# Kernel optimization log

Measured on AMD Instinct MI355X. Metric: run time of the kernel, lower is better.

## Reference

```python
import jax, jax.numpy as jnp
import numpy as np

# IR-Net EDE surrogate-gradient constants (ir_1w1a.IRConv2d defaults)
K = 10.0
T = 0.1
BN_EPS = 1e-5

@jax.custom_vjp
def binary_quantize(x):
    return jnp.sign(x)

def _bq_fwd(x):
    return jnp.sign(x), x

def _bq_bwd(x, g):
    # grad = k * t * (1 - tanh(x*t)^2) * g   (IR-Net BinaryQuantize.backward)
    return (K * T * (1.0 - jnp.tanh(x * T) ** 2) * g,)

binary_quantize.defvjp(_bq_fwd, _bq_bwd)


def setup_inputs() -> dict:
    key = jax.random.key(0)
    k1, k2 = jax.random.split(key, 2)
    return {
        "x": jax.random.normal(k1, (32, 256, 56, 56), dtype=jnp.float32),
        "weight": jax.random.normal(k2, (256, 256, 3, 3), dtype=jnp.float32) * 0.05,
        "gamma": jnp.ones((256,), dtype=jnp.float32),
        "beta": jnp.zeros((256,), dtype=jnp.float32),
    }


def _convalg(x, weight, gamma, beta):
    co = weight.shape[0]
    wf = weight.reshape(co, -1)
    # per-output-channel standardization of weights
    bw = weight - wf.mean(-1).reshape(co, 1, 1, 1)
    std = jnp.std(bw.reshape(co, -1), axis=-1, ddof=1).reshape(co, 1, 1, 1)  # torch unbiased std
    bw = bw / std
    # detached power-of-2 per-channel scale: sw = 2^round(log2(mean|bw|))
    sw = jax.lax.stop_gradient(
        2.0 ** jnp.round(jnp.log2(jnp.abs(bw).reshape(co, -1).mean(-1)))
    ).reshape(co, 1, 1, 1)
    bwq = binary_quantize(bw) * sw   # binarized, scaled weights {-sw, +sw}
    ba = binary_quantize(x)          # binarized activations {-1, +1}
    y = jax.lax.conv_general_dilated(
        ba, bwq,
        window_strides=(1, 1),
        padding=((1, 1), (1, 1)),
        dimension_numbers=("NCHW", "OIHW", "NCHW"),
    )
    # BatchNorm2d, training-mode forward (batch statistics, biased variance)
    mean = y.mean(axis=(0, 2, 3), keepdims=True)
    var = y.var(axis=(0, 2, 3), keepdims=True)
    yn = (y - mean) * jax.lax.rsqrt(var + BN_EPS)
    yn = yn * gamma.reshape(1, -1, 1, 1) + beta.reshape(1, -1, 1, 1)
    # Hardtanh
    return jnp.clip(yn, -1.0, 1.0)


def reference(x, weight, gamma, beta):
    return _convalg(x, weight, gamma, beta)
```

## Files before the change

kernel.cpp:

```cpp
#include <hip/hip_runtime.h>
#include <math.h>

#define HH 56
#define WW 56
#define NB 32
#define CC 256
#define PIX 3136
#define M_TOT 100352
#define PADH 58
#define PADW 58
#define ACTQ_BYTES ((size_t)NB*PADH*PADW*CC)
#define WQ_BYTES ((size_t)9*CC*CC)
#define SBUF_BYTES ((size_t)M_TOT*CC*2)
#define BM 128
#define BN 256

typedef unsigned int u32;
typedef unsigned long long u64;
typedef int v4i __attribute__((ext_vector_type(4)));

typedef const __attribute__((address_space(1))) unsigned int* as1_u32p;
typedef __attribute__((address_space(3))) unsigned int* as3_u32p;
#define GLOAD_LDS16(g, l) \
  __builtin_amdgcn_global_load_lds((as1_u32p)(g), (as3_u32p)(l), 16, 0, 0)

__global__ __launch_bounds__(256) void pack_weights_i8(
    const float* __restrict__ wt, signed char* __restrict__ wq,
    float* __restrict__ swv,
    long long* __restrict__ sumS, long long* __restrict__ sumSS) {
  int co = blockIdx.x;
  int t  = threadIdx.x;
  int lane = t & 63, wid = t >> 6;

  float wv[9];
  const float* wp = wt + ((size_t)co*CC + t)*9;
  double psum = 0.0;
#pragma unroll
  for (int k = 0; k < 9; ++k) { wv[k] = wp[k]; psum += (double)wv[k]; }

  __shared__ double redm[4];
#pragma unroll
  for (int off = 32; off > 0; off >>= 1) psum += __shfl_xor(psum, off);
  if (lane == 0) redm[wid] = psum;
  __syncthreads();
  double mean = (redm[0]+redm[1]+redm[2]+redm[3]) * (1.0/2304.0);

  double pabs = 0.0, psq = 0.0;
#pragma unroll
  for (int k = 0; k < 9; ++k) {
    double d = (double)wv[k] - mean;
    pabs += fabs(d);
    psq  += d*d;
  }
#pragma unroll
  for (int off = 32; off > 0; off >>= 1) {
    pabs += __shfl_xor(pabs, off);
    psq  += __shfl_xor(psq,  off);
  }
  __shared__ double reda[4], redq[4];
  if (lane == 0) { reda[wid] = pabs; redq[wid] = psq; }
  __syncthreads();
  if (t == 0) {
    double sa = reda[0]+reda[1]+reda[2]+reda[3];
    double sq = redq[0]+redq[1]+redq[2]+redq[3];
    double stdv = sqrt(sq / 2303.0);
    double mabs = (sa * (1.0/2304.0)) / stdv;
    swv[co] = (float)exp2(rint(log2(mabs)));
    sumS[co]  = 0;
    sumSS[co] = 0;
  }
#pragma unroll
  for (int k = 0; k < 9; ++k)
    wq[((size_t)k*CC + co)*CC + t] =
        (((double)wv[k] - mean) > 0.0) ? (signed char)1 : (signed char)-1;
}

__global__ __launch_bounds__(256) void pack_acts_i8(
    const float* __restrict__ x, signed char* __restrict__ actq) {
  int n = blockIdx.y, tile = blockIdx.x;
  int lane = threadIdx.x & 63, cw = threadIdx.x >> 6;
  int pp = tile*64 + lane;
  if (pp >= PADH*PADW) return;
  int ph = pp / PADW, pw = pp - ph*PADW;
  signed char* dst = actq + ((size_t)(n*PADH + ph)*PADW + pw)*CC + cw*64;
  if (ph == 0 || ph == PADH-1 || pw == 0 || pw == PADW-1) {
    uint4 z = make_uint4(0u, 0u, 0u, 0u);
#pragma unroll
    for (int q = 0; q < 4; ++q) ((uint4*)dst)[q] = z;
    return;
  }
  int h = ph - 1, w = pw - 1;
  const float* xp = x + ((size_t)(n*CC + cw*64))*PIX + h*WW + w;
  u32 wrd[16];
#pragma unroll
  for (int c16 = 0; c16 < 16; ++c16) {
    u32 v = 0;
#pragma unroll
    for (int b = 0; b < 4; ++b) {
      float f = xp[(size_t)(c16*4 + b)*PIX];
      v |= (f > 0.0f ? 0x01u : 0xFFu) << (8*b);
    }
    wrd[c16] = v;
  }
#pragma unroll
  for (int q = 0; q < 4; ++q)
    ((uint4*)dst)[q] = make_uint4(wrd[4*q], wrd[4*q+1], wrd[4*q+2], wrd[4*q+3]);
}


#define STAGEM(SN, BUF) do {                                              \
    int tn_ = (SN) >> 2, kn_ = (SN) & 3;                                  \
    int aoff_ = ((tn_/3 - 1)*PADW + (tn_%3 - 1))*CC + kn_*64;             \
    int boff_ = tn_*65536 + kn_*64;                                       \
    char* nb_ = (char*)lds + (BUF)*24576;                                 \
    GLOAD_LDS16(pA0 + aoff_, nb_ + ldst);                                 \
    GLOAD_LDS16(pA1 + aoff_, nb_ + 4096 + ldst);                          \
    GLOAD_LDS16(pB0 + boff_, nb_ + 8192 + ldst);                          \
    GLOAD_LDS16(pB1 + boff_, nb_ + 12288 + ldst);                         \
    GLOAD_LDS16(pB2 + boff_, nb_ + 16384 + ldst);                         \
    GLOAD_LDS16(pB3 + boff_, nb_ + 20480 + ldst);                         \
  } while (0)

#define STEPB(S, WTXT, DODMA) do {                                        \
    asm volatile("s_waitcnt " WTXT ::: "memory");                         \
    __builtin_amdgcn_s_barrier();                                         \
    if (DODMA) { STAGEM((S) + 2, ((S) + 2) % 3); }                        \
    const char* cb_ = (const char*)lds + ((S) % 3)*24576;                 \
    v4i af[4], bf[8];                                                     \
    _Pragma("unroll")                                                     \
    for (int i = 0; i < 4; ++i)                                           \
      af[i] = *(const v4i*)(cb_ + (ar0 + i*16 + lm)*64 + rdo);            \
    _Pragma("unroll")                                                     \
    for (int j = 0; j < 8; ++j)                                           \
      bf[j] = *(const v4i*)(cb_ + 8192 + (bc0 + j*16 + lm)*64 + rdo);     \
    __builtin_amdgcn_s_setprio(1);                                        \
    _Pragma("unroll")                                                     \
    for (int i = 0; i < 4; ++i)                                           \
      _Pragma("unroll")                                                   \
      for (int j = 0; j < 8; ++j)                                         \
        acc[i][j] = __builtin_amdgcn_mfma_i32_16x16x64_i8(af[i], bf[j],   \
                                                          acc[i][j], 0, 0, 0); \
    __builtin_amdgcn_s_setprio(0);                                        \
  } while (0)

template <bool S16>
__global__ __launch_bounds__(256, 2) void bconv_mfma(
    const signed char* __restrict__ actq, const signed char* __restrict__ wq,
    short* __restrict__ s16out, float* __restrict__ f32out,
    u64* __restrict__ sumS, u64* __restrict__ sumSS) {
  __shared__ char lds[73728] __attribute__((aligned(16)));
  __shared__ int colS[256], colQ[256];

  int t = threadIdx.x;
  int lane = t & 63, wv = t >> 6;
  int lm = lane & 15, quad = lane >> 4;
  int ar0 = (wv & 1) * 64;
  int bc0 = (wv >> 1) * 128;
  int Mbase = blockIdx.x * BM;

  colS[t] = 0; colQ[t] = 0;

  int r = t >> 2, c16 = t & 3;
  int cs = c16 ^ ((r >> 1) & 3);
  const signed char *pA0, *pA1;
  {
    int P = Mbase + r;
    int n_ = P / PIX, pl_ = P % PIX, h_ = pl_ / WW, w_ = pl_ % WW;
    pA0 = actq + ((size_t)(n_*PADH + h_+1)*PADW + (w_+1))*CC + cs*16;
    P += 64;
    n_ = P / PIX; pl_ = P % PIX; h_ = pl_ / WW; w_ = pl_ % WW;
    pA1 = actq + ((size_t)(n_*PADH + h_+1)*PADW + (w_+1))*CC + cs*16;
  }
  const signed char* pB0 = wq + (size_t)r*CC + cs*16;
  const signed char* pB1 = pB0 +  64*CC;
  const signed char* pB2 = pB0 + 128*CC;
  const signed char* pB3 = pB0 + 192*CC;
  int ldst = t*16;

  int rdo = (quad ^ ((lm >> 1) & 3)) * 16;

  v4i acc[4][8];
#pragma unroll
  for (int i = 0; i < 4; ++i)
#pragma unroll
    for (int j = 0; j < 8; ++j) acc[i][j] = 0;

  STAGEM(0, 0);
  STAGEM(1, 1);

#pragma unroll 1
  for (int s = 0; s < 33; s += 3) {
    STEPB(s,     "vmcnt(6)", true);
    STEPB(s + 1, "vmcnt(6)", true);
    STEPB(s + 2, "vmcnt(6)", true);
  }
  STEPB(33, "vmcnt(6)", true);
  STEPB(34, "vmcnt(6)", false);
  STEPB(35, "vmcnt(0)", false);

  int Sl[8] = {0,0,0,0,0,0,0,0}, Ql[8] = {0,0,0,0,0,0,0,0};
  if (S16) {
    short* tb = s16out + (size_t)blockIdx.x * (BM*BN);
#pragma unroll
    for (int i = 0; i < 4; ++i) {
      int rhat = ar0 + i*16 + quad*4;
#pragma unroll
      for (int j = 0; j < 8; ++j) {
        int colo = bc0 + j*16 + lm;
        v4i a = acc[i][j];
        int2 pk;
        pk.x = (a.x & 0xFFFF) | (a.y << 16);
        pk.y = (a.z & 0xFFFF) | (a.w << 16);
        *(int2*)(tb + (size_t)colo*BM + rhat) = pk;
        Sl[j] += a.x + a.y + a.z + a.w;
        Ql[j] += a.x*a.x + a.y*a.y + a.z*a.z + a.w*a.w;
      }
    }
  } else {
#pragma unroll
    for (int i = 0; i < 4; ++i) {
      int R = Mbase + ar0 + i*16 + quad*4;
      int nR = R / PIX, plR = R % PIX;
#pragma unroll
      for (int j = 0; j < 8; ++j) {
        int colo = bc0 + j*16 + lm;
        v4i a = acc[i][j];
        size_t idx = ((size_t)nR*CC + colo)*PIX + plR;
        *(float4*)(f32out + idx) =
            make_float4((float)a.x, (float)a.y, (float)a.z, (float)a.w);
        Sl[j] += a.x + a.y + a.z + a.w;
        Ql[j] += a.x*a.x + a.y*a.y + a.z*a.z + a.w*a.w;
      }
    }
  }
#pragma unroll
  for (int j = 0; j < 8; ++j) {
    int S = Sl[j], Q = Ql[j];
    S += __shfl_xor(S, 16); S += __shfl_xor(S, 32);
    Q += __shfl_xor(Q, 16); Q += __shfl_xor(Q, 32);
    if (quad == 0) {
      atomicAdd(&colS[bc0 + j*16 + lm], S);
      atomicAdd(&colQ[bc0 + j*16 + lm], Q);
    }
  }
  __syncthreads();
  atomicAdd(&sumS[t], (u64)(long long)colS[t]);
  atomicAdd(&sumSS[t], (u64)(long long)colQ[t]);
}

__global__ void finalize_stats(
    const long long* __restrict__ sumS, const long long* __restrict__ sumSS,
    const float* __restrict__ swv,
    const float* __restrict__ gamma, const float* __restrict__ beta,
    float* __restrict__ AB) {
  int c = threadIdx.x;
  double mu  = (double)sumS[c]  / (double)M_TOT;
  double var = (double)sumSS[c] / (double)M_TOT - mu*mu;
  double sw  = (double)swv[c];
  double inv = 1.0 / sqrt(sw*sw*var + 1e-5);
  double scale = (double)gamma[c] * sw * inv;
  double shift = (double)beta[c] - scale * mu;
  AB[c]      = (float)scale;
  AB[CC + c] = (float)shift;
}

__global__ __launch_bounds__(256) void bn_apply_s16(
    const short* __restrict__ s, float* __restrict__ out,
    const float* __restrict__ AB, int n8) {
  int i = blockIdx.x*256 + threadIdx.x;
  if (i >= n8) return;
  union { int4 v; short sh[8]; } u;
  u.v = ((const int4*)s)[i];
  int base   = i*8;
  int tile   = base >> 15;
  int within = base & 32767;
  int col    = within >> 7;
  int rh     = within & 127;
  int R  = tile*BM + rh;
  int n_ = R / PIX, pl = R % PIX;
  float a = AB[col], b = AB[CC + col];
  float* op = out + ((size_t)n_*CC + col)*PIX + pl;
  float4 o0, o1;
  o0.x = fminf(1.f, fmaxf(-1.f, (float)u.sh[0]*a + b));
  o0.y = fminf(1.f, fmaxf(-1.f, (float)u.sh[1]*a + b));
  o0.z = fminf(1.f, fmaxf(-1.f, (float)u.sh[2]*a + b));
  o0.w = fminf(1.f, fmaxf(-1.f, (float)u.sh[3]*a + b));
  o1.x = fminf(1.f, fmaxf(-1.f, (float)u.sh[4]*a + b));
  o1.y = fminf(1.f, fmaxf(-1.f, (float)u.sh[5]*a + b));
  o1.z = fminf(1.f, fmaxf(-1.f, (float)u.sh[6]*a + b));
  o1.w = fminf(1.f, fmaxf(-1.f, (float)u.sh[7]*a + b));
  ((float4*)op)[0] = o0;
  ((float4*)op)[1] = o1;
}

__global__ __launch_bounds__(256) void bn_apply_f32(
    float* __restrict__ out, const float* __restrict__ AB, int n4) {
  int i = blockIdx.x*256 + threadIdx.x;
  if (i >= n4) return;
  float4 v = ((float4*)out)[i];
  int c = ((i*4) / PIX) & (CC-1);
  float a = AB[c], b = AB[CC + c];
  v.x = fminf(1.f, fmaxf(-1.f, v.x*a + b));
  v.y = fminf(1.f, fmaxf(-1.f, v.y*a + b));
  v.z = fminf(1.f, fmaxf(-1.f, v.z*a + b));
  v.w = fminf(1.f, fmaxf(-1.f, v.w*a + b));
  ((float4*)out)[i] = v;
}

extern "C" void kernel_launch(void* const* d_in, const int* in_sizes, int n_in,
                              void* d_out, int out_size, void* d_ws, size_t ws_size,
                              hipStream_t stream) {
  (void)in_sizes; (void)n_in; (void)out_size;
  const float* x     = (const float*)d_in[0];
  const float* wt    = (const float*)d_in[1];
  const float* gamma = (const float*)d_in[2];
  const float* beta  = (const float*)d_in[3];
  float* out = (float*)d_out;

  char* ws = (char*)d_ws;
  size_t off = 0;
  signed char* actq = (signed char*)(ws + off);
  off += ACTQ_BYTES;             off = (off + 255) & ~(size_t)255;
  signed char* wq = (signed char*)(ws + off);
  off += WQ_BYTES;               off = (off + 255) & ~(size_t)255;
  float* swv = (float*)(ws + off); off += 1024;
  float* AB  = (float*)(ws + off); off += 2048;
  long long* sumS  = (long long*)(ws + off); off += 2048;
  long long* sumSS = (long long*)(ws + off); off += 2048;
  off = (off + 255) & ~(size_t)255;
  short* sbuf = (short*)(ws + off);
  bool s16 = (ws_size >= off + SBUF_BYTES);

  pack_weights_i8<<<256, 256, 0, stream>>>(wt, wq, swv, sumS, sumSS);
  pack_acts_i8<<<dim3(53, NB), 256, 0, stream>>>(x, actq);
  if (s16) {
    bconv_mfma<true><<<dim3(M_TOT/BM, 1), 256, 0, stream>>>(
        actq, wq, sbuf, nullptr, (u64*)sumS, (u64*)sumSS);
  } else {
    bconv_mfma<false><<<dim3(M_TOT/BM, 1), 256, 0, stream>>>(
        actq, wq, nullptr, out, (u64*)sumS, (u64*)sumSS);
  }
  finalize_stats<<<1, 256, 0, stream>>>(sumS, sumSS, swv, gamma, beta, AB);
  if (s16) {
    bn_apply_s16<<<(M_TOT*CC/8 + 255)/256, 256, 0, stream>>>(
        sbuf, out, AB, M_TOT*CC/8);
  } else {
    bn_apply_f32<<<(M_TOT*CC/4 + 255)/256, 256, 0, stream>>>(
        out, AB, M_TOT*CC/4);
  }
}
```

Baseline: 157.9 us.

## Enlarge conv tile to 256x256 with 8 waves and interleaved double-buffer pipeline

Doubles the M tile of the int8 MFMA implicit-GEMM conv to 256 rows with 512 threads (8 waves in a 2x4 grid). The LDS ring changes from triple to double buffering, and A and B staging are split and interleaved with sub-blocks of MFMAs separated by barriers. This aims to raise data reuse per LDS byte and hide global loads behind compute. In exchange it adds many more block-wide barriers per k-step and a full vmcnt(0) drain every iteration, and it updates the bn_apply tile indexing to match.

```diff
diff --git a/kernel.cpp b/kernel.cpp
--- a/kernel.cpp
+++ b/kernel.cpp
@@ -12,7 +12,7 @@
 #define ACTQ_BYTES ((size_t)NB*PADH*PADW*CC)
 #define WQ_BYTES ((size_t)9*CC*CC)
 #define SBUF_BYTES ((size_t)M_TOT*CC*2)
-#define BM 128
+#define BM 256
 #define BN 256
 
 typedef unsigned int u32;
@@ -108,57 +108,22 @@
 }
 
 
-#define STAGEM(SN, BUF) do {                                              \
-    int tn_ = (SN) >> 2, kn_ = (SN) & 3;                                  \
-    int aoff_ = ((tn_/3 - 1)*PADW + (tn_%3 - 1))*CC + kn_*64;             \
-    int boff_ = tn_*65536 + kn_*64;                                       \
-    char* nb_ = (char*)lds + (BUF)*24576;                                 \
-    GLOAD_LDS16(pA0 + aoff_, nb_ + ldst);                                 \
-    GLOAD_LDS16(pA1 + aoff_, nb_ + 4096 + ldst);                          \
-    GLOAD_LDS16(pB0 + boff_, nb_ + 8192 + ldst);                          \
-    GLOAD_LDS16(pB1 + boff_, nb_ + 12288 + ldst);                         \
-    GLOAD_LDS16(pB2 + boff_, nb_ + 16384 + ldst);                         \
-    GLOAD_LDS16(pB3 + boff_, nb_ + 20480 + ldst);                         \
-  } while (0)
-
-#define STEPB(S, WTXT, DODMA) do {                                        \
-    asm volatile("s_waitcnt " WTXT ::: "memory");                         \
-    __builtin_amdgcn_s_barrier();                                         \
-    if (DODMA) { STAGEM((S) + 2, ((S) + 2) % 3); }                        \
-    const char* cb_ = (const char*)lds + ((S) % 3)*24576;                 \
-    v4i af[4], bf[8];                                                     \
-    _Pragma("unroll")                                                     \
-    for (int i = 0; i < 4; ++i)                                           \
-      af[i] = *(const v4i*)(cb_ + (ar0 + i*16 + lm)*64 + rdo);            \
-    _Pragma("unroll")                                                     \
-    for (int j = 0; j < 8; ++j)                                           \
-      bf[j] = *(const v4i*)(cb_ + 8192 + (bc0 + j*16 + lm)*64 + rdo);     \
-    __builtin_amdgcn_s_setprio(1);                                        \
-    _Pragma("unroll")                                                     \
-    for (int i = 0; i < 4; ++i)                                           \
-      _Pragma("unroll")                                                   \
-      for (int j = 0; j < 8; ++j)                                         \
-        acc[i][j] = __builtin_amdgcn_mfma_i32_16x16x64_i8(af[i], bf[j],   \
-                                                          acc[i][j], 0, 0, 0); \
-    __builtin_amdgcn_s_setprio(0);                                        \
-  } while (0)
-
 template <bool S16>
-__global__ __launch_bounds__(256, 2) void bconv_mfma(
+__global__ __launch_bounds__(512, 4) void bconv_mfma(
     const signed char* __restrict__ actq, const signed char* __restrict__ wq,
     short* __restrict__ s16out, float* __restrict__ f32out,
     u64* __restrict__ sumS, u64* __restrict__ sumSS) {
-  __shared__ char lds[73728] __attribute__((aligned(16)));
+  __shared__ char lds[65536] __attribute__((aligned(16)));
   __shared__ int colS[256], colQ[256];
 
   int t = threadIdx.x;
   int lane = t & 63, wv = t >> 6;
   int lm = lane & 15, quad = lane >> 4;
-  int ar0 = (wv & 1) * 64;
-  int bc0 = (wv >> 1) * 128;
+  int wr = wv >> 2;
+  int wc = wv & 3;
   int Mbase = blockIdx.x * BM;
 
-  colS[t] = 0; colQ[t] = 0;
+  if (t < 256) { colS[t] = 0; colQ[t] = 0; }
 
   int r = t >> 2, c16 = t & 3;
   int cs = c16 ^ ((r >> 1) & 3);
@@ -167,46 +132,96 @@
     int P = Mbase + r;
     int n_ = P / PIX, pl_ = P % PIX, h_ = pl_ / WW, w_ = pl_ % WW;
     pA0 = actq + ((size_t)(n_*PADH + h_+1)*PADW + (w_+1))*CC + cs*16;
-    P += 64;
+    P += 128;
     n_ = P / PIX; pl_ = P % PIX; h_ = pl_ / WW; w_ = pl_ % WW;
     pA1 = actq + ((size_t)(n_*PADH + h_+1)*PADW + (w_+1))*CC + cs*16;
   }
   const signed char* pB0 = wq + (size_t)r*CC + cs*16;
-  const signed char* pB1 = pB0 +  64*CC;
-  const signed char* pB2 = pB0 + 128*CC;
-  const signed char* pB3 = pB0 + 192*CC;
+  const signed char* pB1 = pB0 + 128*CC;
   int ldst = t*16;
 
   int rdo = (quad ^ ((lm >> 1) & 3)) * 16;
 
-  v4i acc[4][8];
-#pragma unroll
-  for (int i = 0; i < 4; ++i)
-#pragma unroll
-    for (int j = 0; j < 8; ++j) acc[i][j] = 0;
-
-  STAGEM(0, 0);
-  STAGEM(1, 1);
+  v4i acc[8][4];
+#pragma unroll
+  for (int i = 0; i < 8; ++i)
+#pragma unroll
+    for (int j = 0; j < 4; ++j) acc[i][j] = 0;
+
+#define STAGE_A(SN) do {                                                  \
+    int tn_ = (SN) >> 2, kn_ = (SN) & 3;                                  \
+    int aoff_ = ((tn_/3 - 1)*PADW + (tn_%3 - 1))*CC + kn_*64;             \
+    char* nb_ = (char*)lds + (((SN) & 1) << 15);                          \
+    GLOAD_LDS16(pA0 + aoff_, nb_ + ldst);                                 \
+    GLOAD_LDS16(pA1 + aoff_, nb_ + 8192 + ldst);                          \
+  } while (0)
+#define STAGE_B(SN) do {                                                  \
+    int tn_ = (SN) >> 2, kn_ = (SN) & 3;                                  \
+    int boff_ = tn_*65536 + kn_*64;                                       \
+    char* nb_ = (char*)lds + (((SN) & 1) << 15);                          \
+    GLOAD_LDS16(pB0 + boff_, nb_ + 16384 + ldst);                         \
+    GLOAD_LDS16(pB1 + boff_, nb_ + 24576 + ldst);                         \
+  } while (0)
+#define MFMA8(I0, J0) do {                                                \
+    __builtin_amdgcn_s_setprio(1);                                        \
+    _Pragma("unroll")                                                     \
+    for (int i_ = 0; i_ < 4; ++i_)                                        \
+      _Pragma("unroll")                                                   \
+      for (int j_ = 0; j_ < 2; ++j_)                                      \
+        acc[(I0)+i_][(J0)+j_] = __builtin_amdgcn_mfma_i32_16x16x64_i8(    \
+            af[(I0)+i_], bf[(J0)+j_], acc[(I0)+i_][(J0)+j_], 0, 0, 0);    \
+    __builtin_amdgcn_s_setprio(0);                                        \
+  } while (0)
+
+  STAGE_A(0);
+  STAGE_B(0);
+  asm volatile("s_waitcnt vmcnt(0)" ::: "memory");
+  __builtin_amdgcn_s_barrier();
+  __builtin_amdgcn_sched_barrier(0);
 
 #pragma unroll 1
-  for (int s = 0; s < 33; s += 3) {
-    STEPB(s,     "vmcnt(6)", true);
-    STEPB(s + 1, "vmcnt(6)", true);
-    STEPB(s + 2, "vmcnt(6)", true);
-  }
-  STEPB(33, "vmcnt(6)", true);
-  STEPB(34, "vmcnt(6)", false);
-  STEPB(35, "vmcnt(0)", false);
-
-  int Sl[8] = {0,0,0,0,0,0,0,0}, Ql[8] = {0,0,0,0,0,0,0,0};
+  for (int s = 0; s < 36; ++s) {
+    const char* cb_ = (const char*)lds + ((s & 1) << 15);
+    bool dostage = (s < 35);
+    v4i af[8], bf[4];
+    if (dostage) STAGE_A(s + 1);
+#pragma unroll
+    for (int i = 0; i < 4; ++i)
+      af[i] = *(const v4i*)(cb_ + (wr*128 + i*16 + lm)*64 + rdo);
+#pragma unroll
+    for (int j = 0; j < 2; ++j)
+      bf[j] = *(const v4i*)(cb_ + 16384 + (wc*64 + j*16 + lm)*64 + rdo);
+    __builtin_amdgcn_s_barrier();
+    MFMA8(0, 0);
+    __builtin_amdgcn_s_barrier();
+    if (dostage) STAGE_B(s + 1);
+#pragma unroll
+    for (int j = 2; j < 4; ++j)
+      bf[j] = *(const v4i*)(cb_ + 16384 + (wc*64 + j*16 + lm)*64 + rdo);
+    __builtin_amdgcn_s_barrier();
+    MFMA8(0, 2);
+    __builtin_amdgcn_s_barrier();
+#pragma unroll
+    for (int i = 4; i < 8; ++i)
+      af[i] = *(const v4i*)(cb_ + (wr*128 + i*16 + lm)*64 + rdo);
+    __builtin_amdgcn_s_barrier();
+    MFMA8(4, 0);
+    __builtin_amdgcn_s_barrier();
+    MFMA8(4, 2);
+    asm volatile("s_waitcnt vmcnt(0)" ::: "memory");
+    __builtin_amdgcn_s_barrier();
+    __builtin_amdgcn_sched_barrier(0);
+  }
+
+  int Sl[4] = {0,0,0,0}, Ql[4] = {0,0,0,0};
   if (S16) {
     short* tb = s16out + (size_t)blockIdx.x * (BM*BN);
 #pragma unroll
-    for (int i = 0; i < 4; ++i) {
-      int rhat = ar0 + i*16 + quad*4;
-#pragma unroll
-      for (int j = 0; j < 8; ++j) {
-        int colo = bc0 + j*16 + lm;
+    for (int i = 0; i < 8; ++i) {
+      int rhat = wr*128 + i*16 + quad*4;
+#pragma unroll
+      for (int j = 0; j < 4; ++j) {
+        int colo = wc*64 + j*16 + lm;
         v4i a = acc[i][j];
         int2 pk;
         pk.x = (a.x & 0xFFFF) | (a.y << 16);
@@ -218,12 +233,12 @@
     }
   } else {
 #pragma unroll
-    for (int i = 0; i < 4; ++i) {
-      int R = Mbase + ar0 + i*16 + quad*4;
+    for (int i = 0; i < 8; ++i) {
+      int R = Mbase + wr*128 + i*16 + quad*4;
       int nR = R / PIX, plR = R % PIX;
 #pragma unroll
-      for (int j = 0; j < 8; ++j) {
-        int colo = bc0 + j*16 + lm;
+      for (int j = 0; j < 4; ++j) {
+        int colo = wc*64 + j*16 + lm;
         v4i a = acc[i][j];
         size_t idx = ((size_t)nR*CC + colo)*PIX + plR;
         *(float4*)(f32out + idx) =
@@ -234,18 +249,20 @@
     }
   }
 #pragma unroll
-  for (int j = 0; j < 8; ++j) {
+  for (int j = 0; j < 4; ++j) {
     int S = Sl[j], Q = Ql[j];
     S += __shfl_xor(S, 16); S += __shfl_xor(S, 32);
     Q += __shfl_xor(Q, 16); Q += __shfl_xor(Q, 32);
     if (quad == 0) {
-      atomicAdd(&colS[bc0 + j*16 + lm], S);
-      atomicAdd(&colQ[bc0 + j*16 + lm], Q);
+      atomicAdd(&colS[wc*64 + j*16 + lm], S);
+      atomicAdd(&colQ[wc*64 + j*16 + lm], Q);
     }
   }
   __syncthreads();
-  atomicAdd(&sumS[t], (u64)(long long)colS[t]);
-  atomicAdd(&sumSS[t], (u64)(long long)colQ[t]);
+  if (t < 256) {
+    atomicAdd(&sumS[t], (u64)(long long)colS[t]);
+    atomicAdd(&sumSS[t], (u64)(long long)colQ[t]);
+  }
 }
 
 __global__ void finalize_stats(
@@ -272,10 +289,10 @@
   union { int4 v; short sh[8]; } u;
   u.v = ((const int4*)s)[i];
   int base   = i*8;
-  int tile   = base >> 15;
-  int within = base & 32767;
-  int col    = within >> 7;
-  int rh     = within & 127;
+  int tile   = base >> 16;
+  int within = base & 65535;
+  int col    = within >> 8;
+  int rh     = within & 255;
   int R  = tile*BM + rh;
   int n_ = R / PIX, pl = R % PIX;
   float a = AB[col], b = AB[CC + col];
@@ -334,10 +351,10 @@
   pack_weights_i8<<<256, 256, 0, stream>>>(wt, wq, swv, sumS, sumSS);
   pack_acts_i8<<<dim3(53, NB), 256, 0, stream>>>(x, actq);
   if (s16) {
-    bconv_mfma<true><<<dim3(M_TOT/BM, 1), 256, 0, stream>>>(
+    bconv_mfma<true><<<dim3(M_TOT/BM, 1), 512, 0, stream>>>(
         actq, wq, sbuf, nullptr, (u64*)sumS, (u64*)sumSS);
   } else {
-    bconv_mfma<false><<<dim3(M_TOT/BM, 1), 256, 0, stream>>>(
+    bconv_mfma<false><<<dim3(M_TOT/BM, 1), 512, 0, stream>>>(
         actq, wq, nullptr, out, (u64*)sumS, (u64*)sumSS);
   }
   finalize_stats<<<1, 256, 0, stream>>>(sumS, sumSS, swv, gamma, beta, AB);
```

After: 557.6 us. 253% more time.
